# Performance work log

Measured on AMD Instinct MI355X. Metric: run time of the kernel, lower is better.

## Reference

```python
import jax, jax.numpy as jnp
import numpy as np

N = 100000   # particles
D = 100      # grid cells per dimension


def setup_inputs() -> dict:
    rng = np.random.default_rng(0)
    d = 0.05  # cell_size in source
    # distinct cells (module assumes one particle per cell)
    cells = rng.choice(D ** 3, size=N, replace=False)
    cz = cells // (D * D)
    cy = (cells // D) % D
    cx = cells % D
    jit = rng.uniform(-0.3, 0.3, size=(3, N)) * d  # |jitter| < 0.5*d keeps round(pos/d)==cell
    x = cx * d + jit[0]
    y = cy * d + jit[1]
    z = cz * d + jit[2]
    v = rng.standard_normal((3, N)) * 0.1
    kn = 60000.0
    restitution = 0.5
    alpha = -np.log(restitution) / np.pi
    gamma = alpha / np.sqrt(alpha ** 2 + 1.0)
    rho_p = 2700.0
    particle_mass = 4.0 / 3.0 * 3.1415 * d ** 3 * rho_p
    eta = 2.0 * gamma * np.sqrt(kn * particle_mass / 2.0)
    return {
        "compressed_x_grid": jnp.asarray(x, jnp.float32),
        "compressed_y_grid": jnp.asarray(y, jnp.float32),
        "compressed_z_grid": jnp.asarray(z, jnp.float32),
        "compressed_vx_grid": jnp.asarray(v[0], jnp.float32),
        "compressed_vy_grid": jnp.asarray(v[1], jnp.float32),
        "compressed_vz_grid": jnp.asarray(v[2], jnp.float32),
        "d": float(d),
        "kn": float(kn),
        "damping_coefficient_Eta": float(eta),
        "friction_coefficient": 0.5,
        "dt": 0.001,
        "input_shape": D,
        "filter_size": 5,
    }


def _forces(x, y, z, vx, vy, vz, d, kn, eta, grid_dim, filter_size):
    n = x.shape[0]
    eps = 1e-4
    # cell indices exactly as in the torch code: round(pos/d)
    cx = jnp.round(x / d).astype(jnp.int32)
    cy = jnp.round(y / d).astype(jnp.int32)
    cz = jnp.round(z / d).astype(jnp.int32)
    # dense particle-index grid; -1 = empty (replaces mask + particle_number_tensor)
    idx = -jnp.ones((grid_dim, grid_dim, grid_dim), jnp.int32)
    idx = idx.at[cz, cy, cx].set(jnp.arange(n, dtype=jnp.int32))
    # all filter_size^3 roll offsets; torch.roll wraps, so use modular indexing
    r = filter_size // 2
    ar = jnp.arange(-r, r + 1)
    off = jnp.stack(jnp.meshgrid(ar, ar, ar, indexing="ij"), axis=-1).reshape(-1, 3)  # [K,3] (sz,sy,sx)
    # pair (A at cell c) with (B at cell c - s): mask_contact_A==2 <=> occ[c] & occ[c-s]
    nz = (cz[:, None] - off[None, :, 0]) % grid_dim  # [N,K]
    ny = (cy[:, None] - off[None, :, 1]) % grid_dim
    nx = (cx[:, None] - off[None, :, 2]) % grid_dim
    B = idx[nz, ny, nx]                                   # [N,K] neighbor particle id or -1
    me = jnp.arange(n, dtype=jnp.int32)[:, None]
    valid = (B >= 0) & (B != me)                          # filters empty cells and self pairs (A != B)
    Bs = jnp.where(valid, B, 0)
    dxp = x[:, None] - x[Bs]
    dyp = y[:, None] - y[Bs]
    dzp = z[:, None] - z[Bs]
    dvx = vx[:, None] - vx[Bs]
    dvy = vy[:, None] - vy[Bs]
    dvz = vz[:, None] - vz[Bs]
    dist = jnp.sqrt(dxp * dxp + dyp * dyp + dzp * dzp)
    denom = jnp.maximum(eps, dist)
    contact = valid & (dist < 2.0 * d)
    # spring (collision) force on A, aggregated over neighbors (row-sum == scatter_add to A)
    coef = jnp.where(contact, kn * (dist - 2.0 * d) / denom, 0.0)
    fx_c = (coef * dxp).sum(axis=1)
    fy_c = (coef * dyp).sum(axis=1)
    fz_c = (coef * dzp).sum(axis=1)
    # normal damping force
    vn = (dvx * dxp + dvy * dyp + dvz * dzp) / denom
    dcoef = jnp.where(contact, eta * vn / denom, 0.0)
    fx_d = (dcoef * dxp).sum(axis=1)
    fy_d = (dcoef * dyp).sum(axis=1)
    fz_d = (dcoef * dzp).sum(axis=1)
    return jnp.stack([fx_c, fy_c, fz_c, fx_d, fy_d, fz_d])  # [6, N]


def reference(compressed_x_grid, compressed_y_grid, compressed_z_grid, compressed_vx_grid, compressed_vy_grid, compressed_vz_grid, d, kn, damping_coefficient_Eta, friction_coefficient, dt, input_shape, filter_size):
    return _forces(compressed_x_grid, compressed_y_grid, compressed_z_grid,
                   compressed_vx_grid, compressed_vy_grid, compressed_vz_grid,
                   d, kn, damping_coefficient_Eta, input_shape, filter_size)
```

## Files before the change

### kernel.cpp

```cpp
#include <hip/hip_runtime.h>

static const int DG = 100;
static const int PGD = DG + 4;
static const int PCELLS = PGD * PGD * PGD;

static const int TX = 10, TY = 10, TZ = 5;
static const int HX = TX + 4, HY = TY + 4, HZ = TZ + 4;
static const int HPLANE = HX * HY;
static const int HCELLS = HPLANE * HZ;
static const int TCELLS = TX * TY * TZ;
static const int NTX = DG / TX, NTY = DG / TY, NTZ = DG / TZ;
static const int NTILES = NTX * NTY * NTZ;


__global__ __launch_bounds__(256) void scatter_kernel(
    const float* __restrict__ x, const float* __restrict__ y, const float* __restrict__ z,
    const float* __restrict__ vx, const float* __restrict__ vy, const float* __restrict__ vz,
    const float* __restrict__ dptr,
    float4* __restrict__ posid, float4* __restrict__ vel4, int n)
{
    int i = blockIdx.x * blockDim.x + threadIdx.x;
    if (i >= n) return;
    float inv_d = 1.0f / dptr[0];
    float xi = x[i], yi = y[i], zi = z[i];
    int cx = (int)roundf(xi * inv_d);
    int cy = (int)roundf(yi * inv_d);
    int cz = (int)roundf(zi * inv_d);
    int cell = ((cz + 2) * PGD + (cy + 2)) * PGD + (cx + 2);
    float4 pv;
    pv.x = xi; pv.y = yi; pv.z = zi; pv.w = __int_as_float(i);
    posid[cell] = pv;
    float4 vv;
    vv.x = vx[i]; vv.y = vy[i]; vv.z = vz[i]; vv.w = 0.0f;
    vel4[i] = vv;
}

__global__ __launch_bounds__(256) void force_kernel(
    const float* __restrict__ dptr, const float* __restrict__ knptr,
    const float* __restrict__ etaptr,
    const float4* __restrict__ posid, const float4* __restrict__ vel4,
    float* __restrict__ out, int n)
{
    __shared__ float4 tile[HCELLS];
    __shared__ unsigned short list[TCELLS];
    __shared__ int cnt;

    int b = blockIdx.x;
    int txi = b % NTX;
    int tyi = (b / NTX) % NTY;
    int tzi = b / (NTX * NTY);
    int ox = txi * TX, oy = tyi * TY, oz = tzi * TZ;

    int t = threadIdx.x;
    if (t == 0) cnt = 0;

    for (int l = t; l < HCELLS; l += 256) {
        int lz = l / HPLANE;
        int r  = l - lz * HPLANE;
        int ly = r / HX;
        int lx = r - ly * HX;
        tile[l] = posid[((oz + lz) * PGD + (oy + ly)) * PGD + (ox + lx)];
    }
    __syncthreads();

    for (int i = t; i < TCELLS; i += 256) {
        int iz = i / (TX * TY);
        int r  = i - iz * (TX * TY);
        int iy = r / TX;
        int ix = r - iy * TX;
        int l = (iz + 2) * HPLANE + (iy + 2) * HX + (ix + 2);
        if (__float_as_int(tile[l].w) >= 0) {
            int pos = atomicAdd(&cnt, 1);
            list[pos] = (unsigned short)l;
        }
    }
    __syncthreads();
    int nOcc = cnt;
    if (nOcc == 0) return;

    float d   = dptr[0];
    float kn  = knptr[0];
    float eta = etaptr[0];
    float two_d = 2.0f * d;

    int lane = t & 63;
    int wv   = t >> 6;
    int sub  = lane >> 5;
    int l32  = lane & 31;

    int offs[4];
    #pragma unroll
    for (int j = 0; j < 4; ++j) {
        int k = l32 + 32 * j;
        if (k > 124) k = 62;
        int sz = k / 25; int rr = k - sz * 25; int sy = rr / 5; int sx = rr - sy * 5;
        offs[j] = (sz - 2) * HPLANE + (sy - 2) * HX + (sx - 2);
    }

    int nRounds = (nOcc + 7) >> 3;
    for (int rd = 0; rd < nRounds; ++rd) {
        int iw = rd * 8 + wv * 2 + sub;
        bool active = (iw < nOcc);
        int il = active ? iw : (nOcc - 1);
        int c = list[il];
        float4 self = tile[c];
        int pid = __float_as_int(self.w);
        float4 pvel = vel4[pid];

        float fxc = 0.f, fyc = 0.f, fzc = 0.f;
        float fxd = 0.f, fyd = 0.f, fzd = 0.f;

        #pragma unroll
        for (int j = 0; j < 4; ++j) {
            float4 nb = tile[c + offs[j]];
            int B = __float_as_int(nb.w);
            if (B >= 0 && B != pid) {
                float dxp = self.x - nb.x;
                float dyp = self.y - nb.y;
                float dzp = self.z - nb.z;
                float d2 = dxp * dxp + dyp * dyp + dzp * dzp;
                float dist = __builtin_amdgcn_sqrtf(d2);
                if (dist < two_d) {
                    float denom   = fmaxf(1e-4f, dist);
                    float inv_den = __builtin_amdgcn_rcpf(denom);
                    float coef = kn * (dist - two_d) * inv_den;
                    fxc += coef * dxp; fyc += coef * dyp; fzc += coef * dzp;
                    float4 bv = vel4[B];
                    float dvxp = pvel.x - bv.x;
                    float dvyp = pvel.y - bv.y;
                    float dvzp = pvel.z - bv.z;
                    float vn    = (dvxp * dxp + dvyp * dyp + dvzp * dzp) * inv_den;
                    float dcoef = eta * vn * inv_den;
                    fxd += dcoef * dxp; fyd += dcoef * dyp; fzd += dcoef * dzp;
                }
            }
        }

        #pragma unroll
        for (int off = 16; off >= 1; off >>= 1) {
            fxc += __shfl_xor(fxc, off, 64);
            fyc += __shfl_xor(fyc, off, 64);
            fzc += __shfl_xor(fzc, off, 64);
            fxd += __shfl_xor(fxd, off, 64);
            fyd += __shfl_xor(fyd, off, 64);
            fzd += __shfl_xor(fzd, off, 64);
        }

        if (active && l32 < 6) {
            float v = (l32 == 0) ? fxc
                    : (l32 == 1) ? fyc
                    : (l32 == 2) ? fzc
                    : (l32 == 3) ? fxd
                    : (l32 == 4) ? fyd : fzd;
            out[l32 * n + pid] = v;
        }
    }
}

extern "C" void kernel_launch(void* const* d_in, const int* in_sizes, int n_in,
                              void* d_out, int out_size, void* d_ws, size_t ws_size,
                              hipStream_t stream)
{
    const float* x     = (const float*)d_in[0];
    const float* y     = (const float*)d_in[1];
    const float* z     = (const float*)d_in[2];
    const float* vx    = (const float*)d_in[3];
    const float* vy    = (const float*)d_in[4];
    const float* vz    = (const float*)d_in[5];
    const float* dptr  = (const float*)d_in[6];
    const float* knptr = (const float*)d_in[7];
    const float* etap  = (const float*)d_in[8];
    int n = in_sizes[0];

    float4* posid = (float4*)d_ws;
    float4* vel4  = (float4*)((char*)d_ws + (size_t)PCELLS * sizeof(float4));

    hipMemsetAsync(posid, 0xFF, (size_t)PCELLS * sizeof(float4), stream);

    int sblocks = (n + 255) / 256;
    scatter_kernel<<<sblocks, 256, 0, stream>>>(x, y, z, vx, vy, vz, dptr,
                                                posid, vel4, n);

    force_kernel<<<NTILES, 256, 0, stream>>>(dptr, knptr, etap,
                                             posid, vel4, (float*)d_out, n);
}
```

Baseline: 134.6 us.

## Use 512-thread blocks and 16-lane groups per particle in force kernel

The force kernel now launches 512 threads per block, and each particle's 125 neighbor offsets are split across 16 lanes with 8 offsets per lane, where before it was 32 lanes with 4 each. Each round then handles 32 particles instead of 8, so a tile of about 50 occupied cells needs two rounds instead of seven, and the shuffle reduction is one step shorter. The occupancy scan is now a single pass because TCELLS is 500, which fits under 512. The cost is more registers per thread for the unrolled 8-neighbor loop, more idle lanes in the second round, and larger blocks that may lower the number of resident blocks per CU.

After: 120.9 us. -10.2%, faster.

```diff
diff --git a/kernel.cpp b/kernel.cpp
--- a/kernel.cpp
+++ b/kernel.cpp
@@ -11,6 +11,8 @@
 static const int TCELLS = TX * TY * TZ;
 static const int NTX = DG / TX, NTY = DG / TY, NTZ = DG / TZ;
 static const int NTILES = NTX * NTY * NTZ;
+
+static const int BLK = 512;
 
 
 __global__ __launch_bounds__(256) void scatter_kernel(
@@ -35,7 +37,7 @@
     vel4[i] = vv;
 }
 
-__global__ __launch_bounds__(256) void force_kernel(
+__global__ __launch_bounds__(BLK) void force_kernel(
     const float* __restrict__ dptr, const float* __restrict__ knptr,
     const float* __restrict__ etaptr,
     const float4* __restrict__ posid, const float4* __restrict__ vel4,
@@ -54,7 +56,7 @@
     int t = threadIdx.x;
     if (t == 0) cnt = 0;
 
-    for (int l = t; l < HCELLS; l += 256) {
+    for (int l = t; l < HCELLS; l += BLK) {
         int lz = l / HPLANE;
         int r  = l - lz * HPLANE;
         int ly = r / HX;
@@ -63,9 +65,9 @@
     }
     __syncthreads();
 
-    for (int i = t; i < TCELLS; i += 256) {
-        int iz = i / (TX * TY);
-        int r  = i - iz * (TX * TY);
+    if (t < TCELLS) {
+        int iz = t / (TX * TY);
+        int r  = t - iz * (TX * TY);
         int iy = r / TX;
         int ix = r - iy * TX;
         int l = (iz + 2) * HPLANE + (iy + 2) * HX + (ix + 2);
@@ -85,21 +87,21 @@
 
     int lane = t & 63;
     int wv   = t >> 6;
-    int sub  = lane >> 5;
-    int l32  = lane & 31;
+    int sub  = lane >> 4;
+    int l16  = lane & 15;
 
-    int offs[4];
+    int offs[8];
     #pragma unroll
-    for (int j = 0; j < 4; ++j) {
-        int k = l32 + 32 * j;
+    for (int j = 0; j < 8; ++j) {
+        int k = l16 + 16 * j;
         if (k > 124) k = 62;
         int sz = k / 25; int rr = k - sz * 25; int sy = rr / 5; int sx = rr - sy * 5;
         offs[j] = (sz - 2) * HPLANE + (sy - 2) * HX + (sx - 2);
     }
 
-    int nRounds = (nOcc + 7) >> 3;
+    int nRounds = (nOcc + 31) >> 5;
     for (int rd = 0; rd < nRounds; ++rd) {
-        int iw = rd * 8 + wv * 2 + sub;
+        int iw = rd * 32 + wv * 4 + sub;
         bool active = (iw < nOcc);
         int il = active ? iw : (nOcc - 1);
         int c = list[il];
@@ -111,7 +113,7 @@
         float fxd = 0.f, fyd = 0.f, fzd = 0.f;
 
         #pragma unroll
-        for (int j = 0; j < 4; ++j) {
+        for (int j = 0; j < 8; ++j) {
             float4 nb = tile[c + offs[j]];
             int B = __float_as_int(nb.w);
             if (B >= 0 && B != pid) {
@@ -137,7 +139,7 @@
         }
 
         #pragma unroll
-        for (int off = 16; off >= 1; off >>= 1) {
+        for (int off = 8; off >= 1; off >>= 1) {
             fxc += __shfl_xor(fxc, off, 64);
             fyc += __shfl_xor(fyc, off, 64);
             fzc += __shfl_xor(fzc, off, 64);
@@ -146,13 +148,13 @@
             fzd += __shfl_xor(fzd, off, 64);
         }
 
-        if (active && l32 < 6) {
-            float v = (l32 == 0) ? fxc
-                    : (l32 == 1) ? fyc
-                    : (l32 == 2) ? fzc
-                    : (l32 == 3) ? fxd
-                    : (l32 == 4) ? fyd : fzd;
-            out[l32 * n + pid] = v;
+        if (active && l16 < 6) {
+            float v = (l16 == 0) ? fxc
+                    : (l16 == 1) ? fyc
+                    : (l16 == 2) ? fzc
+                    : (l16 == 3) ? fxd
+                    : (l16 == 4) ? fyd : fzd;
+            out[l16 * n + pid] = v;
         }
     }
 }
@@ -181,6 +183,6 @@
     scatter_kernel<<<sblocks, 256, 0, stream>>>(x, y, z, vx, vy, vz, dptr,
                                                 posid, vel4, n);
 
-    force_kernel<<<NTILES, 256, 0, stream>>>(dptr, knptr, etap,
+    force_kernel<<<NTILES, BLK, 0, stream>>>(dptr, knptr, etap,
                                              posid, vel4, (float*)d_out, n);
 }
```
